# Kernel optimization log

Hardware: AMD Instinct MI355X
Metric: run time of the kernel (lower is better)

## Reference

```python
import jax, jax.numpy as jnp
import numpy as np

E = 6        # num_experts
C = 256      # embed_dim (expert in_channels)
HID = 256    # mlp_dim (expert hidden_channels)
META = 9
GATE_H = 128
BN_EPS = 1e-5  # torch BatchNorm2d default


def _conv(x, w):
    # x: [1,Cin,H,W], w: [Cout,Cin,3,3] -> [1,Cout,H,W], padding=1
    return jax.lax.conv_general_dilated(
        x, w, window_strides=(1, 1), padding=((1, 1), (1, 1)),
        dimension_numbers=("NCHW", "OIHW", "NCHW"))


def _bn(x, mean, var, gamma, beta):
    # inference-mode BatchNorm2d over channel dim
    scale = gamma * jax.lax.rsqrt(var + BN_EPS)
    return (x - mean[None, :, None, None]) * scale[None, :, None, None] + beta[None, :, None, None]


def setup_inputs() -> dict:
    key = jax.random.key(0)
    ks = jax.random.split(key, 20)
    B, H, W = 16, 64, 64
    f32 = jnp.float32
    return {
        "moe_c4": jax.random.normal(ks[0], (B, C, H, W), f32),
        "meta": jax.random.normal(ks[1], (B, META), f32),
        # Gate MLP: Linear(9,128) -> ReLU -> Linear(128,6)
        "gate_w1": jax.random.normal(ks[2], (META, GATE_H), f32) * 0.3,
        "gate_b1": jnp.zeros((GATE_H,), f32),
        "gate_w2": jax.random.normal(ks[3], (GATE_H, E), f32) * 0.1,
        "gate_b2": jnp.zeros((E,), f32),
        # Expert conv1: Conv2d(C, HID, 3) + BN(HID), stacked over experts
        "conv1_w": jax.random.normal(ks[4], (E, HID, C, 3, 3), f32) * 0.02,
        "conv1_b": jnp.zeros((E, HID), f32),
        "bn1_g": jnp.ones((E, HID), f32) + 0.1 * jax.random.normal(ks[5], (E, HID), f32),
        "bn1_b": 0.1 * jax.random.normal(ks[6], (E, HID), f32),
        "bn1_m": 0.1 * jax.random.normal(ks[7], (E, HID), f32),
        "bn1_v": jax.random.uniform(ks[8], (E, HID), f32) + 0.5,
        # Expert conv2: Conv2d(HID, C, 3) + BN(C)
        "conv2_w": jax.random.normal(ks[9], (E, C, HID, 3, 3), f32) * 0.02,
        "conv2_b": jnp.zeros((E, C), f32),
        "bn2_g": jnp.ones((E, C), f32) + 0.1 * jax.random.normal(ks[10], (E, C), f32),
        "bn2_b": 0.1 * jax.random.normal(ks[11], (E, C), f32),
        "bn2_m": 0.1 * jax.random.normal(ks[12], (E, C), f32),
        "bn2_v": jax.random.uniform(ks[13], (E, C), f32) + 0.5,
    }


def reference(moe_c4, meta, gate_w1, gate_b1, gate_w2, gate_b2,
              conv1_w, conv1_b, bn1_g, bn1_b, bn1_m, bn1_v,
              conv2_w, conv2_b, bn2_g, bn2_b, bn2_m, bn2_v):
    # --- Gate: MLP -> softmax -> top-1 routing ---
    h = jax.nn.relu(meta @ gate_w1 + gate_b1)
    gate_probs = jax.nn.softmax(h @ gate_w2 + gate_b2, axis=-1)  # [B,E]
    top1 = jnp.argmax(gate_probs, axis=-1)                        # [B]

    # --- Dispatch: gather each sample's expert params, run one conv stack per sample ---
    def one(x, w1, b1, g1, be1, m1, v1, w2, b2, g2, be2, m2, v2):
        y = _conv(x[None], w1) + b1[None, :, None, None]
        y = jax.nn.relu(_bn(y, m1, v1, g1, be1))
        y = _conv(y, w2) + b2[None, :, None, None]
        y = jax.nn.relu(_bn(y, m2, v2, g2, be2))
        return y[0]

    out = jax.vmap(one)(
        moe_c4,
        conv1_w[top1], conv1_b[top1], bn1_g[top1], bn1_b[top1], bn1_m[top1], bn1_v[top1],
        conv2_w[top1], conv2_b[top1], bn2_g[top1], bn2_b[top1], bn2_m[top1], bn2_v[top1])

    # --- Load-balance loss (torch.std is unbiased -> ddof=1) ---
    importance = gate_probs.sum(axis=0) / (gate_probs.sum() + 1e-8)
    balance_loss = jnp.std(importance, ddof=1)
    return out, balance_loss
```

## Files before the change

kernel.cpp:

```cpp
#include <hip/hip_runtime.h>
#include <hip/hip_bf16.h>

typedef unsigned short u16;
typedef unsigned int u32;
typedef __attribute__((ext_vector_type(8))) short short8_v;
typedef __attribute__((ext_vector_type(4))) float float4_v;

__device__ __forceinline__ u16 f2bf(float f) {
  u32 u = __float_as_uint(f);
  return (u16)((u + 0x7fffu + ((u >> 16) & 1u)) >> 16);
}

__device__ __forceinline__ void gl_lds16(const void* g, void* l) {
  __builtin_amdgcn_global_load_lds(
      (const __attribute__((address_space(1))) u32*)g,
      (__attribute__((address_space(3))) u32*)l, 16, 0, 0);
}

__device__ __forceinline__ void stage_tile_1024(const char* src, char* dst, int wid, int lane) {
  const int u0 = wid * 256;
  #pragma unroll
  for (int i = 0; i < 4; ++i) {
    int u = u0 + i * 64 + lane;
    int cl = u >> 2;
    int qs = (u & 3) ^ ((u >> 3) & 3);
    gl_lds16(src + (size_t)cl * 512 + qs * 16, dst + (size_t)(u0 + i * 64) * 16);
  }
}
__device__ __forceinline__ void stage_tile_B(const char* src, char* dst, int wid, int lane) {
  stage_tile_1024(src, dst, wid, lane);
  if (wid == 0) {
    int u = 1024 + lane;
    int du = u >> 2;
    int qs = (u & 3) ^ ((u >> 3) & 3);
    gl_lds16(src + (size_t)du * 512 + qs * 16, dst + (size_t)1024 * 16);
  }
}

__global__ void gate_fold_kernel(const float* __restrict__ meta,
                                 const float* __restrict__ gw1, const float* __restrict__ gb1,
                                 const float* __restrict__ gw2, const float* __restrict__ gb2,
                                 const float* __restrict__ c1b, const float* __restrict__ g1,
                                 const float* __restrict__ be1, const float* __restrict__ m1,
                                 const float* __restrict__ v1,
                                 const float* __restrict__ c2b, const float* __restrict__ g2,
                                 const float* __restrict__ be2, const float* __restrict__ m2,
                                 const float* __restrict__ v2,
                                 float* __restrict__ fold1, float* __restrict__ fold2,
                                 int* __restrict__ top1, float* __restrict__ loss_out) {
  const int tid = threadIdx.x;
  __shared__ float probs[16][6];

  for (int t = tid; t < 3072; t += 1024) {
    int conv = t >= 1536 ? 1 : 0;
    int r = t - (conv ? 1536 : 0);
    if (conv == 0) {
      float scale = g1[r] * rsqrtf(v1[r] + 1e-5f);
      float shift = (c1b[r] - m1[r]) * scale + be1[r];
      fold1[r * 2] = scale; fold1[r * 2 + 1] = shift;
    } else {
      float scale = g2[r] * rsqrtf(v2[r] + 1e-5f);
      float shift = (c2b[r] - m2[r]) * scale + be2[r];
      fold2[r * 2] = scale; fold2[r * 2 + 1] = shift;
    }
  }

  const int b = tid >> 6, lane = tid & 63;
  float h0 = gb1[lane], h1 = gb1[lane + 64];
  #pragma unroll
  for (int i = 0; i < 9; ++i) {
    float m = meta[b * 9 + i];
    h0 += m * gw1[i * 128 + lane];
    h1 += m * gw1[i * 128 + lane + 64];
  }
  h0 = fmaxf(h0, 0.f); h1 = fmaxf(h1, 0.f);
  float v[6];
  #pragma unroll
  for (int k = 0; k < 6; ++k)
    v[k] = h0 * gw2[lane * 6 + k] + h1 * gw2[(lane + 64) * 6 + k];
  #pragma unroll
  for (int off = 32; off >= 1; off >>= 1)
    #pragma unroll
    for (int k = 0; k < 6; ++k) v[k] += __shfl_xor(v[k], off, 64);
  if (lane == 0) {
    float lg[6];
    #pragma unroll
    for (int k = 0; k < 6; ++k) lg[k] = v[k] + gb2[k];
    float m = lg[0];
    for (int k = 1; k < 6; ++k) m = fmaxf(m, lg[k]);
    float s = 0.f, p[6];
    for (int k = 0; k < 6; ++k) { p[k] = expf(lg[k] - m); s += p[k]; }
    int best = 0; float bm = p[0];
    for (int k = 1; k < 6; ++k) if (p[k] > bm) { bm = p[k]; best = k; }
    top1[b] = best;
    for (int k = 0; k < 6; ++k) probs[b][k] = p[k] / s;
  }
  __syncthreads();
  if (tid == 0) {
    float col[6] = {0, 0, 0, 0, 0, 0}, tot = 0.f;
    for (int bb = 0; bb < 16; ++bb)
      for (int k = 0; k < 6; ++k) col[k] += probs[bb][k];
    for (int k = 0; k < 6; ++k) tot += col[k];
    float imp[6], mean = 0.f;
    for (int k = 0; k < 6; ++k) { imp[k] = col[k] / (tot + 1e-8f); mean += imp[k]; }
    mean *= (1.f / 6.f);
    float var = 0.f;
    for (int k = 0; k < 6; ++k) { float d = imp[k] - mean; var += d * d; }
    loss_out[0] = sqrtf(var * 0.2f);
  }
}

__global__ void prep_kernel(const float* __restrict__ w1, const float* __restrict__ w2,
                            u16* __restrict__ w1t, u16* __restrict__ w2t,
                            const float* __restrict__ x, u16* __restrict__ xpt,
                            u16* __restrict__ hpt) {
  const int tid = threadIdx.x;
  __shared__ u16 tile[64 * 258];
  const int bx = blockIdx.x;

  if (bx < 3072) {
    float* buf = (float*)tile;
    const int conv = bx >= 1536 ? 1 : 0;
    const int r = bx - (conv ? 1536 : 0);
    const int e = r >> 8, co = r & 255;
    const float* src = (conv ? w2 : w1) + (size_t)r * 2304;
    u16* wdst = conv ? w2t : w1t;
    const float4* s4 = (const float4*)src;
    for (int k = tid; k < 576; k += 256) ((float4*)buf)[k] = s4[k];
    __syncthreads();
    for (int j = tid; j < 288; j += 256) {
      int tap = j >> 5, ci0 = (j & 31) * 8;
      u16 v[8];
      #pragma unroll
      for (int i = 0; i < 8; ++i) v[i] = f2bf(buf[(ci0 + i) * 9 + tap]);
      int4 pk;
      pk.x = (int)((u32)v[0] | ((u32)v[1] << 16));
      pk.y = (int)((u32)v[2] | ((u32)v[3] << 16));
      pk.z = (int)((u32)v[4] | ((u32)v[5] << 16));
      pk.w = (int)((u32)v[6] | ((u32)v[7] << 16));
      *(int4*)(wdst + (((size_t)e * 9 + tap) * 256 + co) * 256 + ci0) = pk;
    }
    return;
  }
  if (bx >= 4096) {
    int t = (bx - 4096) * 256 + tid;
    int buf = t / (16 * 260 * 32);
    int r = t % (16 * 260 * 32);
    int b = r / (260 * 32);
    int r2 = r % (260 * 32);
    int idx = r2 >> 5, part = r2 & 31;
    int rc;
    if (idx < 66) rc = idx;
    else if (idx < 132) rc = 65 * 66 + (idx - 66);
    else { int rem = idx - 132; rc = (1 + (rem >> 1)) * 66 + (rem & 1) * 65; }
    u16* base = buf ? hpt : xpt;
    int4 z = {0, 0, 0, 0};
    *(int4*)(base + ((size_t)b * 4356 + rc) * 256 + part * 8) = z;
    return;
  }
  const int blk = bx - 3072;
  const int b = blk >> 6, r = blk & 63;
  const int cg = tid & 15, ci_g = tid >> 4;
  const float4* xb4 = (const float4*)(x + ((size_t)b * 256) * 4096 + r * 64);
  #pragma unroll
  for (int k = 0; k < 16; ++k) {
    int ci = k * 16 + ci_g;
    float4 v = xb4[(size_t)ci * 1024 + cg];
    tile[(cg * 4 + 0) * 258 + ci] = f2bf(v.x);
    tile[(cg * 4 + 1) * 258 + ci] = f2bf(v.y);
    tile[(cg * 4 + 2) * 258 + ci] = f2bf(v.z);
    tile[(cg * 4 + 3) * 258 + ci] = f2bf(v.w);
  }
  __syncthreads();
  u16* dstb = xpt + ((size_t)b * 4356 + (size_t)(r + 1) * 66 + 1) * 256;
  #pragma unroll
  for (int it = 0; it < 8; ++it) {
    int chunk = it * 256 + tid;
    int cc = chunk >> 5, part = chunk & 31;
    const u32* lp = (const u32*)(tile + cc * 258 + part * 8);
    int4 vv = {(int)lp[0], (int)lp[1], (int)lp[2], (int)lp[3]};
    *(int4*)(dstb + (size_t)cc * 256 + part * 8) = vv;
  }
}

template <int MODE>
__global__ __launch_bounds__(256, 2) void conv_mfma_kernel(
    const u16* __restrict__ src, const u16* __restrict__ wt,
    const int* __restrict__ top1, const float* __restrict__ fold,
    float* __restrict__ outF, u16* __restrict__ outH) {
  __shared__ char Ab[2 * 16384];
  __shared__ char Bb[2 * 17408];
  const int tid = threadIdx.x;
  const int lane = tid & 63;
  const int wid = tid >> 6;
  const int wr = wid >> 1, wc = wid & 1;
  const int orig = blockIdx.x;
  const int swz = (orig & 7) * 64 + (orig >> 3);
  const int ptile = swz & 31, b = swz >> 5;
  const int e = top1[b];

  const char* srcB0 = (const char*)src + ((size_t)b * 4356 + (size_t)ptile * 132) * 512;
  const char* wA0 = (const char*)wt + (size_t)e * 9 * 65536 * 2;

  float4_v acc[8][4];
  #pragma unroll
  for (int m = 0; m < 8; ++m)
    #pragma unroll
    for (int n = 0; n < 4; ++n)
      acc[m][n] = (float4_v){0.f, 0.f, 0.f, 0.f};

  stage_tile_1024(wA0, Ab, wid, lane);
  stage_tile_B(srcB0, Bb, wid, lane);
  asm volatile("s_waitcnt vmcnt(0)" ::: "memory");
  __builtin_amdgcn_s_barrier();

  for (int chunk = 0; chunk < 8; ++chunk) {
    #pragma unroll
    for (int tap = 0; tap < 9; ++tap) {
      const int cur = (chunk + tap) & 1;
      if (!(chunk == 7 && tap == 8)) {
        const int ntap = (tap == 8) ? 0 : tap + 1;
        const int nchunk = (tap == 8) ? chunk + 1 : chunk;
        stage_tile_1024(wA0 + (size_t)ntap * 131072 + nchunk * 64,
                        Ab + (cur ^ 1) * 16384, wid, lane);
      }
      if (tap == 0 && chunk < 7)
        stage_tile_B(srcB0 + (chunk + 1) * 64, Bb + ((chunk + 1) & 1) * 17408, wid, lane);

      const char* aB = Ab + cur * 16384;
      const char* bB = Bb + (chunk & 1) * 17408;
      const int kh = tap / 3, kw = tap % 3;
      short8_v bv[4];
      #pragma unroll
      for (int n = 0; n < 4; ++n) {
        int pt = wc * 64 + n * 16 + (lane & 15);
        int rc = ((pt >> 6) + kh) * 66 + (pt & 63) + kw;
        int slot = (lane >> 4) ^ ((rc >> 1) & 3);
        bv[n] = *(const short8_v*)(bB + rc * 64 + slot * 16);
      }
      short8_v av[8];
      #pragma unroll
      for (int m = 0; m < 8; ++m) {
        int cl = wr * 128 + m * 16 + (lane & 15);
        int slot = (lane >> 4) ^ ((cl >> 1) & 3);
        av[m] = *(const short8_v*)(aB + cl * 64 + slot * 16);
      }
      #pragma unroll
      for (int m = 0; m < 8; ++m)
        #pragma unroll
        for (int n = 0; n < 4; ++n)
          acc[m][n] = __builtin_amdgcn_mfma_f32_16x16x32_bf16(av[m], bv[n], acc[m][n], 0, 0, 0);
      asm volatile("s_waitcnt vmcnt(0)" ::: "memory");
      __builtin_amdgcn_s_barrier();
    }
  }

  const float* fe = fold + (size_t)e * 512;
  #pragma unroll
  for (int m = 0; m < 8; ++m) {
    const int cb = wr * 128 + m * 16 + ((lane >> 4) << 2);
    float sc0 = fe[(cb + 0) * 2], sh0 = fe[(cb + 0) * 2 + 1];
    float sc1 = fe[(cb + 1) * 2], sh1 = fe[(cb + 1) * 2 + 1];
    float sc2 = fe[(cb + 2) * 2], sh2 = fe[(cb + 2) * 2 + 1];
    float sc3 = fe[(cb + 3) * 2], sh3 = fe[(cb + 3) * 2 + 1];
    #pragma unroll
    for (int n = 0; n < 4; ++n) {
      const int pt = ptile * 128 + wc * 64 + n * 16 + (lane & 15);
      float v0 = fmaxf(acc[m][n][0] * sc0 + sh0, 0.f);
      float v1 = fmaxf(acc[m][n][1] * sc1 + sh1, 0.f);
      float v2 = fmaxf(acc[m][n][2] * sc2 + sh2, 0.f);
      float v3 = fmaxf(acc[m][n][3] * sc3 + sh3, 0.f);
      if (MODE == 1) {
        const size_t rc = (size_t)((pt >> 6) + 1) * 66 + (pt & 63) + 1;
        uint2 pk;
        pk.x = (u32)f2bf(v0) | ((u32)f2bf(v1) << 16);
        pk.y = (u32)f2bf(v2) | ((u32)f2bf(v3) << 16);
        *(uint2*)(outH + ((size_t)b * 4356 + rc) * 256 + cb) = pk;
      } else {
        float* ob = outF + (size_t)b * 1048576;
        ob[(size_t)(cb + 0) * 4096 + pt] = v0;
        ob[(size_t)(cb + 1) * 4096 + pt] = v1;
        ob[(size_t)(cb + 2) * 4096 + pt] = v2;
        ob[(size_t)(cb + 3) * 4096 + pt] = v3;
      }
    }
  }
}

extern "C" void kernel_launch(void* const* d_in, const int* in_sizes, int n_in,
                              void* d_out, int out_size, void* d_ws, size_t ws_size,
                              hipStream_t stream) {
  const float* x    = (const float*)d_in[0];
  const float* meta = (const float*)d_in[1];
  const float* gw1  = (const float*)d_in[2];
  const float* gb1  = (const float*)d_in[3];
  const float* gw2  = (const float*)d_in[4];
  const float* gb2  = (const float*)d_in[5];
  const float* c1w  = (const float*)d_in[6];
  const float* c1b  = (const float*)d_in[7];
  const float* bn1g = (const float*)d_in[8];
  const float* bn1b = (const float*)d_in[9];
  const float* bn1m = (const float*)d_in[10];
  const float* bn1v = (const float*)d_in[11];
  const float* c2w  = (const float*)d_in[12];
  const float* c2b  = (const float*)d_in[13];
  const float* bn2g = (const float*)d_in[14];
  const float* bn2b = (const float*)d_in[15];
  const float* bn2m = (const float*)d_in[16];
  const float* bn2v = (const float*)d_in[17];

  char* ws = (char*)d_ws;
  u16* xpt   = (u16*)(ws);
  u16* hpt   = (u16*)(ws + 35684352);
  u16* w1t   = (u16*)(ws + 71368704);
  u16* w2t   = (u16*)(ws + 78446592);
  float* fold1 = (float*)(ws + 85524480);
  float* fold2 = (float*)(ws + 85536768);
  int* top1  = (int*)(ws + 85549056);

  float* outF = (float*)d_out;
  float* loss = outF + 16777216;

  hipLaunchKernelGGL(gate_fold_kernel, dim3(1), dim3(1024), 0, stream,
                     meta, gw1, gb1, gw2, gb2,
                     c1b, bn1g, bn1b, bn1m, bn1v, c2b, bn2g, bn2b, bn2m, bn2v,
                     fold1, fold2, top1, loss);
  hipLaunchKernelGGL(prep_kernel, dim3(5136), dim3(256), 0, stream,
                     c1w, c2w, w1t, w2t, x, xpt, hpt);
  hipLaunchKernelGGL((conv_mfma_kernel<1>), dim3(512), dim3(256), 0, stream,
                     xpt, w1t, top1, fold1, (float*)nullptr, hpt);
  hipLaunchKernelGGL((conv_mfma_kernel<2>), dim3(512), dim3(256), 0, stream,
                     hpt, w2t, top1, fold2, outF, (u16*)nullptr);
}
```

Measured before the change: 348.5 us.

## Merge gate into prep kernel and drop double-buffered LDS staging in conv

Folds the single-block gate/BN-fold kernel into the prep kernel as an extra block, removing one launch. In the conv kernel, the ping-pong double buffering of the A and B LDS tiles is replaced by single buffers loaded synchronously between two __syncthreads per tap. This halves LDS use, which may allow more resident blocks, and lowers register pressure by loading A fragments one at a time. The cost is that global-to-LDS loads no longer overlap with the MFMA work, which is likely to expose memory latency on every tap.

```diff
diff --git a/kernel.cpp b/kernel.cpp
--- a/kernel.cpp
+++ b/kernel.cpp
@@ -17,106 +17,24 @@
       (__attribute__((address_space(3))) u32*)l, 16, 0, 0);
 }
 
-__device__ __forceinline__ void stage_tile_1024(const char* src, char* dst, int wid, int lane) {
-  const int u0 = wid * 256;
-  #pragma unroll
-  for (int i = 0; i < 4; ++i) {
-    int u = u0 + i * 64 + lane;
-    int cl = u >> 2;
-    int qs = (u & 3) ^ ((u >> 3) & 3);
-    gl_lds16(src + (size_t)cl * 512 + qs * 16, dst + (size_t)(u0 + i * 64) * 16);
-  }
-}
-__device__ __forceinline__ void stage_tile_B(const char* src, char* dst, int wid, int lane) {
-  stage_tile_1024(src, dst, wid, lane);
-  if (wid == 0) {
-    int u = 1024 + lane;
-    int du = u >> 2;
-    int qs = (u & 3) ^ ((u >> 3) & 3);
-    gl_lds16(src + (size_t)du * 512 + qs * 16, dst + (size_t)1024 * 16);
-  }
-}
-
-__global__ void gate_fold_kernel(const float* __restrict__ meta,
-                                 const float* __restrict__ gw1, const float* __restrict__ gb1,
-                                 const float* __restrict__ gw2, const float* __restrict__ gb2,
-                                 const float* __restrict__ c1b, const float* __restrict__ g1,
-                                 const float* __restrict__ be1, const float* __restrict__ m1,
-                                 const float* __restrict__ v1,
-                                 const float* __restrict__ c2b, const float* __restrict__ g2,
-                                 const float* __restrict__ be2, const float* __restrict__ m2,
-                                 const float* __restrict__ v2,
-                                 float* __restrict__ fold1, float* __restrict__ fold2,
-                                 int* __restrict__ top1, float* __restrict__ loss_out) {
+__global__ void prep_all_kernel(const float* __restrict__ w1, const float* __restrict__ w2,
+                                u16* __restrict__ w1t, u16* __restrict__ w2t,
+                                const float* __restrict__ x, u16* __restrict__ xpt,
+                                u16* __restrict__ hpt,
+                                const float* __restrict__ meta,
+                                const float* __restrict__ gw1, const float* __restrict__ gb1,
+                                const float* __restrict__ gw2, const float* __restrict__ gb2,
+                                const float* __restrict__ c1b, const float* __restrict__ g1,
+                                const float* __restrict__ be1, const float* __restrict__ m1,
+                                const float* __restrict__ v1,
+                                const float* __restrict__ c2b, const float* __restrict__ g2,
+                                const float* __restrict__ be2, const float* __restrict__ m2,
+                                const float* __restrict__ v2,
+                                float* __restrict__ fold1, float* __restrict__ fold2,
+                                int* __restrict__ top1, float* __restrict__ loss_out) {
   const int tid = threadIdx.x;
-  __shared__ float probs[16][6];
-
-  for (int t = tid; t < 3072; t += 1024) {
-    int conv = t >= 1536 ? 1 : 0;
-    int r = t - (conv ? 1536 : 0);
-    if (conv == 0) {
-      float scale = g1[r] * rsqrtf(v1[r] + 1e-5f);
-      float shift = (c1b[r] - m1[r]) * scale + be1[r];
-      fold1[r * 2] = scale; fold1[r * 2 + 1] = shift;
-    } else {
-      float scale = g2[r] * rsqrtf(v2[r] + 1e-5f);
-      float shift = (c2b[r] - m2[r]) * scale + be2[r];
-      fold2[r * 2] = scale; fold2[r * 2 + 1] = shift;
-    }
-  }
-
-  const int b = tid >> 6, lane = tid & 63;
-  float h0 = gb1[lane], h1 = gb1[lane + 64];
-  #pragma unroll
-  for (int i = 0; i < 9; ++i) {
-    float m = meta[b * 9 + i];
-    h0 += m * gw1[i * 128 + lane];
-    h1 += m * gw1[i * 128 + lane + 64];
-  }
-  h0 = fmaxf(h0, 0.f); h1 = fmaxf(h1, 0.f);
-  float v[6];
-  #pragma unroll
-  for (int k = 0; k < 6; ++k)
-    v[k] = h0 * gw2[lane * 6 + k] + h1 * gw2[(lane + 64) * 6 + k];
-  #pragma unroll
-  for (int off = 32; off >= 1; off >>= 1)
-    #pragma unroll
-    for (int k = 0; k < 6; ++k) v[k] += __shfl_xor(v[k], off, 64);
-  if (lane == 0) {
-    float lg[6];
-    #pragma unroll
-    for (int k = 0; k < 6; ++k) lg[k] = v[k] + gb2[k];
-    float m = lg[0];
-    for (int k = 1; k < 6; ++k) m = fmaxf(m, lg[k]);
-    float s = 0.f, p[6];
-    for (int k = 0; k < 6; ++k) { p[k] = expf(lg[k] - m); s += p[k]; }
-    int best = 0; float bm = p[0];
-    for (int k = 1; k < 6; ++k) if (p[k] > bm) { bm = p[k]; best = k; }
-    top1[b] = best;
-    for (int k = 0; k < 6; ++k) probs[b][k] = p[k] / s;
-  }
-  __syncthreads();
-  if (tid == 0) {
-    float col[6] = {0, 0, 0, 0, 0, 0}, tot = 0.f;
-    for (int bb = 0; bb < 16; ++bb)
-      for (int k = 0; k < 6; ++k) col[k] += probs[bb][k];
-    for (int k = 0; k < 6; ++k) tot += col[k];
-    float imp[6], mean = 0.f;
-    for (int k = 0; k < 6; ++k) { imp[k] = col[k] / (tot + 1e-8f); mean += imp[k]; }
-    mean *= (1.f / 6.f);
-    float var = 0.f;
-    for (int k = 0; k < 6; ++k) { float d = imp[k] - mean; var += d * d; }
-    loss_out[0] = sqrtf(var * 0.2f);
-  }
-}
-
-__global__ void prep_kernel(const float* __restrict__ w1, const float* __restrict__ w2,
-                            u16* __restrict__ w1t, u16* __restrict__ w2t,
-                            const float* __restrict__ x, u16* __restrict__ xpt,
-                            u16* __restrict__ hpt) {
-  const int tid = threadIdx.x;
+  const int bx = blockIdx.x;
   __shared__ u16 tile[64 * 258];
-  const int bx = blockIdx.x;
 
   if (bx < 3072) {
     float* buf = (float*)tile;
@@ -142,7 +60,33 @@
     }
     return;
   }
-  if (bx >= 4096) {
+  if (bx < 4096) {
+    const int blk = bx - 3072;
+    const int b = blk >> 6, r = blk & 63;
+    const int cg = tid & 15, ci_g = tid >> 4;
+    const float4* xb4 = (const float4*)(x + ((size_t)b * 256) * 4096 + r * 64);
+    #pragma unroll
+    for (int k = 0; k < 16; ++k) {
+      int ci = k * 16 + ci_g;
+      float4 v = xb4[(size_t)ci * 1024 + cg];
+      tile[(cg * 4 + 0) * 258 + ci] = f2bf(v.x);
+      tile[(cg * 4 + 1) * 258 + ci] = f2bf(v.y);
+      tile[(cg * 4 + 2) * 258 + ci] = f2bf(v.z);
+      tile[(cg * 4 + 3) * 258 + ci] = f2bf(v.w);
+    }
+    __syncthreads();
+    u16* dstb = xpt + ((size_t)b * 4356 + (size_t)(r + 1) * 66 + 1) * 256;
+    #pragma unroll
+    for (int it = 0; it < 8; ++it) {
+      int chunk = it * 256 + tid;
+      int cc = chunk >> 5, part = chunk & 31;
+      const u32* lp = (const u32*)(tile + cc * 258 + part * 8);
+      int4 vv = {(int)lp[0], (int)lp[1], (int)lp[2], (int)lp[3]};
+      *(int4*)(dstb + (size_t)cc * 256 + part * 8) = vv;
+    }
+    return;
+  }
+  if (bx < 5136) {
     int t = (bx - 4096) * 256 + tid;
     int buf = t / (16 * 260 * 32);
     int r = t % (16 * 260 * 32);
@@ -158,28 +102,70 @@
     *(int4*)(base + ((size_t)b * 4356 + rc) * 256 + part * 8) = z;
     return;
   }
-  const int blk = bx - 3072;
-  const int b = blk >> 6, r = blk & 63;
-  const int cg = tid & 15, ci_g = tid >> 4;
-  const float4* xb4 = (const float4*)(x + ((size_t)b * 256) * 4096 + r * 64);
-  #pragma unroll
-  for (int k = 0; k < 16; ++k) {
-    int ci = k * 16 + ci_g;
-    float4 v = xb4[(size_t)ci * 1024 + cg];
-    tile[(cg * 4 + 0) * 258 + ci] = f2bf(v.x);
-    tile[(cg * 4 + 1) * 258 + ci] = f2bf(v.y);
-    tile[(cg * 4 + 2) * 258 + ci] = f2bf(v.z);
-    tile[(cg * 4 + 3) * 258 + ci] = f2bf(v.w);
+
+  float* probs = (float*)tile;
+  for (int t = tid; t < 3072; t += 256) {
+    int conv = t >= 1536 ? 1 : 0;
+    int r = t - (conv ? 1536 : 0);
+    if (conv == 0) {
+      float scale = g1[r] * rsqrtf(v1[r] + 1e-5f);
+      float shift = (c1b[r] - m1[r]) * scale + be1[r];
+      fold1[r * 2] = scale; fold1[r * 2 + 1] = shift;
+    } else {
+      float scale = g2[r] * rsqrtf(v2[r] + 1e-5f);
+      float shift = (c2b[r] - m2[r]) * scale + be2[r];
+      fold2[r * 2] = scale; fold2[r * 2 + 1] = shift;
+    }
+  }
+  const int wid = tid >> 6, lane = tid & 63;
+  const float b1a = gb1[lane], b1b = gb1[lane + 64];
+  const float w2a0 = gw2[lane * 6 + 0], w2a1 = gw2[lane * 6 + 1], w2a2 = gw2[lane * 6 + 2];
+  const float w2a3 = gw2[lane * 6 + 3], w2a4 = gw2[lane * 6 + 4], w2a5 = gw2[lane * 6 + 5];
+  const float w2b0 = gw2[(lane + 64) * 6 + 0], w2b1 = gw2[(lane + 64) * 6 + 1], w2b2 = gw2[(lane + 64) * 6 + 2];
+  const float w2b3 = gw2[(lane + 64) * 6 + 3], w2b4 = gw2[(lane + 64) * 6 + 4], w2b5 = gw2[(lane + 64) * 6 + 5];
+  for (int s = 0; s < 4; ++s) {
+    const int b = wid * 4 + s;
+    float h0 = b1a, h1 = b1b;
+    #pragma unroll
+    for (int i = 0; i < 9; ++i) {
+      float m = meta[b * 9 + i];
+      h0 += m * gw1[i * 128 + lane];
+      h1 += m * gw1[i * 128 + lane + 64];
+    }
+    h0 = fmaxf(h0, 0.f); h1 = fmaxf(h1, 0.f);
+    float v[6];
+    v[0] = h0 * w2a0 + h1 * w2b0; v[1] = h0 * w2a1 + h1 * w2b1; v[2] = h0 * w2a2 + h1 * w2b2;
+    v[3] = h0 * w2a3 + h1 * w2b3; v[4] = h0 * w2a4 + h1 * w2b4; v[5] = h0 * w2a5 + h1 * w2b5;
+    #pragma unroll
+    for (int off = 32; off >= 1; off >>= 1)
+      #pragma unroll
+      for (int k = 0; k < 6; ++k) v[k] += __shfl_xor(v[k], off, 64);
+    if (lane == 0) {
+      float lg[6];
+      #pragma unroll
+      for (int k = 0; k < 6; ++k) lg[k] = v[k] + gb2[k];
+      float m = lg[0];
+      for (int k = 1; k < 6; ++k) m = fmaxf(m, lg[k]);
+      float sum = 0.f, p[6];
+      for (int k = 0; k < 6; ++k) { p[k] = expf(lg[k] - m); sum += p[k]; }
+      int best = 0; float bm = p[0];
+      for (int k = 1; k < 6; ++k) if (p[k] > bm) { bm = p[k]; best = k; }
+      top1[b] = best;
+      for (int k = 0; k < 6; ++k) probs[b * 6 + k] = p[k] / sum;
+    }
   }
   __syncthreads();
-  u16* dstb = xpt + ((size_t)b * 4356 + (size_t)(r + 1) * 66 + 1) * 256;
-  #pragma unroll
-  for (int it = 0; it < 8; ++it) {
-    int chunk = it * 256 + tid;
-    int cc = chunk >> 5, part = chunk & 31;
-    const u32* lp = (const u32*)(tile + cc * 258 + part * 8);
-    int4 vv = {(int)lp[0], (int)lp[1], (int)lp[2], (int)lp[3]};
-    *(int4*)(dstb + (size_t)cc * 256 + part * 8) = vv;
+  if (tid == 0) {
+    float col[6] = {0, 0, 0, 0, 0, 0}, tot = 0.f;
+    for (int bb = 0; bb < 16; ++bb)
+      for (int k = 0; k < 6; ++k) col[k] += probs[bb * 6 + k];
+    for (int k = 0; k < 6; ++k) tot += col[k];
+    float imp[6], mean = 0.f;
+    for (int k = 0; k < 6; ++k) { imp[k] = col[k] / (tot + 1e-8f); mean += imp[k]; }
+    mean *= (1.f / 6.f);
+    float var = 0.f;
+    for (int k = 0; k < 6; ++k) { float d = imp[k] - mean; var += d * d; }
+    loss_out[0] = sqrtf(var * 0.2f);
   }
 }
 
@@ -188,8 +174,8 @@
     const u16* __restrict__ src, const u16* __restrict__ wt,
     const int* __restrict__ top1, const float* __restrict__ fold,
     float* __restrict__ outF, u16* __restrict__ outH) {
-  __shared__ char Ab[2 * 16384];
-  __shared__ char Bb[2 * 17408];
+  __shared__ char Ab[16384];
+  __shared__ char Bb[17408];
   const int tid = threadIdx.x;
   const int lane = tid & 63;
   const int wid = tid >> 6;
@@ -209,26 +195,40 @@
     for (int n = 0; n < 4; ++n)
       acc[m][n] = (float4_v){0.f, 0.f, 0.f, 0.f};
 
-  stage_tile_1024(wA0, Ab, wid, lane);
-  stage_tile_B(srcB0, Bb, wid, lane);
-  asm volatile("s_waitcnt vmcnt(0)" ::: "memory");
-  __builtin_amdgcn_s_barrier();
-
   for (int chunk = 0; chunk < 8; ++chunk) {
     #pragma unroll
     for (int tap = 0; tap < 9; ++tap) {
-      const int cur = (chunk + tap) & 1;
-      if (!(chunk == 7 && tap == 8)) {
-        const int ntap = (tap == 8) ? 0 : tap + 1;
-        const int nchunk = (tap == 8) ? chunk + 1 : chunk;
-        stage_tile_1024(wA0 + (size_t)ntap * 131072 + nchunk * 64,
-                        Ab + (cur ^ 1) * 16384, wid, lane);
-      }
-      if (tap == 0 && chunk < 7)
-        stage_tile_B(srcB0 + (chunk + 1) * 64, Bb + ((chunk + 1) & 1) * 17408, wid, lane);
-
-      const char* aB = Ab + cur * 16384;
-      const char* bB = Bb + (chunk & 1) * 17408;
+      __syncthreads();
+      if (tap == 0) {
+        const char* sB = srcB0 + chunk * 64;
+        const int u0 = wid * 256;
+        #pragma unroll
+        for (int i = 0; i < 4; ++i) {
+          int u = u0 + i * 64 + lane;
+          int du = u >> 2;
+          int qs = (u & 3) ^ ((u >> 3) & 3);
+          gl_lds16(sB + (size_t)du * 512 + qs * 16, Bb + (size_t)(u0 + i * 64) * 16);
+        }
+        if (wid == 0) {
+          int u = 1024 + lane;
+          int du = u >> 2;
+          int qs = (u & 3) ^ ((u >> 3) & 3);
+          gl_lds16(sB + (size_t)du * 512 + qs * 16, Bb + 1024 * 16);
+        }
+      }
+      {
+        const char* sA = wA0 + (size_t)tap * 131072 + chunk * 64;
+        const int u0 = wid * 256;
+        #pragma unroll
+        for (int i = 0; i < 4; ++i) {
+          int u = u0 + i * 64 + lane;
+          int cl = u >> 2;
+          int qs = (u & 3) ^ ((u >> 3) & 3);
+          gl_lds16(sA + (size_t)cl * 512 + qs * 16, Ab + (size_t)(u0 + i * 64) * 16);
+        }
+      }
+      __syncthreads();
+
       const int kh = tap / 3, kw = tap % 3;
       short8_v bv[4];
       #pragma unroll
@@ -236,22 +236,17 @@
         int pt = wc * 64 + n * 16 + (lane & 15);
         int rc = ((pt >> 6) + kh) * 66 + (pt & 63) + kw;
         int slot = (lane >> 4) ^ ((rc >> 1) & 3);
-        bv[n] = *(const short8_v*)(bB + rc * 64 + slot * 16);
-      }
-      short8_v av[8];
+        bv[n] = *(const short8_v*)(Bb + rc * 64 + slot * 16);
+      }
       #pragma unroll
       for (int m = 0; m < 8; ++m) {
         int cl = wr * 128 + m * 16 + (lane & 15);
         int slot = (lane >> 4) ^ ((cl >> 1) & 3);
-        av[m] = *(const short8_v*)(aB + cl * 64 + slot * 16);
-      }
-      #pragma unroll
-      for (int m = 0; m < 8; ++m)
+        short8_v avm = *(const short8_v*)(Ab + cl * 64 + slot * 16);
         #pragma unroll
         for (int n = 0; n < 4; ++n)
-          acc[m][n] = __builtin_amdgcn_mfma_f32_16x16x32_bf16(av[m], bv[n], acc[m][n], 0, 0, 0);
-      asm volatile("s_waitcnt vmcnt(0)" ::: "memory");
-      __builtin_amdgcn_s_barrier();
+          acc[m][n] = __builtin_amdgcn_mfma_f32_16x16x32_bf16(avm, bv[n], acc[m][n], 0, 0, 0);
+      }
     }
   }
 
@@ -321,12 +316,11 @@
   float* outF = (float*)d_out;
   float* loss = outF + 16777216;
 
-  hipLaunchKernelGGL(gate_fold_kernel, dim3(1), dim3(1024), 0, stream,
+  hipLaunchKernelGGL(prep_all_kernel, dim3(5137), dim3(256), 0, stream,
+                     c1w, c2w, w1t, w2t, x, xpt, hpt,
                      meta, gw1, gb1, gw2, gb2,
                      c1b, bn1g, bn1b, bn1m, bn1v, c2b, bn2g, bn2b, bn2m, bn2v,
                      fold1, fold2, top1, loss);
-  hipLaunchKernelGGL(prep_kernel, dim3(5136), dim3(256), 0, stream,
-                     c1w, c2w, w1t, w2t, x, xpt, hpt);
   hipLaunchKernelGGL((conv_mfma_kernel<1>), dim3(512), dim3(256), 0, stream,
                      xpt, w1t, top1, fold1, (float*)nullptr, hpt);
   hipLaunchKernelGGL((conv_mfma_kernel<2>), dim3(512), dim3(256), 0, stream,
```

Measured after the change: 327.6 us. 1.06x faster.
